# Kernel optimization log

Measured on AMD Instinct MI355X. Metric: run time of the kernel, lower is better.

The kernel has to match this reference:

```python
import jax, jax.numpy as jnp
import numpy as np

NUM_HEADS = 10
FEATURE_DIM = 200
HEAD_DIM = FEATURE_DIM // NUM_HEADS  # 20


def setup_inputs() -> dict:
    key = jax.random.key(0)
    k0, k1, k2, k3 = jax.random.split(key, 4)
    B, H, F, D = 128, 128, 8, FEATURE_DIM
    x = jax.random.normal(k0, (B, H, F, D), dtype=jnp.float32)
    wq = 0.02 * jax.random.normal(k1, (D, NUM_HEADS * HEAD_DIM), dtype=jnp.float32)
    wk = 0.02 * jax.random.normal(k2, (D, NUM_HEADS * HEAD_DIM), dtype=jnp.float32)
    wv = 0.02 * jax.random.normal(k3, (D, NUM_HEADS * HEAD_DIM), dtype=jnp.float32)
    return {"history_embedding_vec": x, "wq": wq, "wk": wk, "wv": wv}


def reference(history_embedding_vec, wq, wk, wv):
    B, H, F, D = history_embedding_vec.shape  # (batch, history_len, feature_num, feature_dim)
    nh, hd = NUM_HEADS, HEAD_DIM
    # Faithful to torch .view: a raw row-major memory reshape (mixes dims, not a transpose)
    x = history_embedding_vec.reshape(B * F, H, D)
    q = (x @ wq).reshape(B * F, H, nh, hd).transpose(0, 2, 1, 3)  # (BF, nh, H, hd)
    k = (x @ wk).reshape(B * F, H, nh, hd).transpose(0, 2, 1, 3)
    v = (x @ wv).reshape(B * F, H, nh, hd).transpose(0, 2, 1, 3)
    scale = 1.0 / jnp.sqrt(jnp.float32(hd))
    scores = jnp.einsum('bhsd,bhtd->bhst', q, k) * scale  # (BF, nh, H, H)
    attention_weights = jax.nn.softmax(scores, axis=-1)
    out = jnp.einsum('bhst,bhtd->bshd', attention_weights, v).reshape(B, F, H, nh * hd)
    # Original re-uses wq (reshaped, but nh*hd == D so identical) for output projection
    out = (out @ wq.reshape(nh * hd, D)).reshape(B, F, H, D)
    return (attention_weights, out)
```

## Files before the change

### kernel.cpp

```cpp
#include <hip/hip_runtime.h>

typedef __bf16 bf16x8 __attribute__((ext_vector_type(8)));
typedef float f32x4 __attribute__((ext_vector_type(4)));

__device__ __forceinline__ unsigned short f2b(float f) {
  union { float f; unsigned u; } v; v.f = f;
  unsigned u = v.u;
  u = (u + 0x7fffu + ((u >> 16) & 1u)) >> 16;
  return (unsigned short)u;
}
__device__ __forceinline__ void lds_load16(void* lds, const void* g) {
  __builtin_amdgcn_global_load_lds(
      (const __attribute__((address_space(1))) unsigned int*)g,
      (__attribute__((address_space(3))) unsigned int*)lds, 16, 0, 0);
}

__global__ __launch_bounds__(256) void cvt_x_kernel(const float* __restrict__ x,
                                                    unsigned short* __restrict__ xb) {
  size_t i = (size_t)blockIdx.x * 256 + threadIdx.x;
  const float4* xp = (const float4*)(x + i * 8);
  float4 a = xp[0], b = xp[1];
  uint4 o;
  o.x = (unsigned)f2b(a.x) | ((unsigned)f2b(a.y) << 16);
  o.y = (unsigned)f2b(a.z) | ((unsigned)f2b(a.w) << 16);
  o.z = (unsigned)f2b(b.x) | ((unsigned)f2b(b.y) << 16);
  o.w = (unsigned)f2b(b.z) | ((unsigned)f2b(b.w) << 16);
  *(uint4*)(xb + i * 8) = o;
}

__global__ __launch_bounds__(256) void build_wt_kernel(const float* __restrict__ wq,
                                                       const float* __restrict__ wk,
                                                       const float* __restrict__ wv,
                                                       unsigned short* __restrict__ wt) {
  int i = blockIdx.x * 256 + threadIdx.x;
  int n = i / 224, k = i - n * 224;
  float val = 0.f;
  if (n < 600 && k < 200) {
    const float* src = (n < 200) ? wq : ((n < 400) ? wk : wv);
    val = src[k * 200 + (n % 200)];
  }
  wt[i] = f2b(val);
}

__global__ __launch_bounds__(256, 3) void gemm_kernel(
    const unsigned short* __restrict__ A, long Astride,
    const unsigned short* __restrict__ Bt,
    unsigned short* __restrict__ Cb, float* __restrict__ Cf,
    long Cstride, int Ncols, int permuteQKV) {
  __shared__ unsigned short sA[2][128 * 32];
  __shared__ unsigned short sB[2][128 * 32];
  int nb = blockIdx.x, mb = blockIdx.y;
  long mBase = (long)mb * 128;
  int nBase = nb * 128;
  int tid = threadIdx.x;
  int lane = tid & 63, w = tid >> 6;
  int wm = w & 1, wn = w >> 1;
  int frow = lane & 15, fch = lane >> 4;

  int chunk0 = w * 64 + lane;
  int row0 = chunk0 >> 2, cs0 = chunk0 & 3;
  int cg0 = cs0 ^ ((row0 >> 1) & 3);
  int chunk1 = 256 + chunk0;
  int row1 = chunk1 >> 2, cs1 = chunk1 & 3;
  int cg1 = cs1 ^ ((row1 >> 1) & 3);

  f32x4 acc[4][4] = {};

#define STAGE(buf, k0)                                                          \
  do {                                                                          \
    lds_load16(&sA[buf][(w * 64) * 8], A + (mBase + row0) * Astride + (k0) + cg0 * 8); \
    lds_load16(&sB[buf][(w * 64) * 8], Bt + (long)(nBase + row0) * 224 + (k0) + cg0 * 8); \
    lds_load16(&sA[buf][(256 + w * 64) * 8], A + (mBase + row1) * Astride + (k0) + cg1 * 8); \
    lds_load16(&sB[buf][(256 + w * 64) * 8], Bt + (long)(nBase + row1) * 224 + (k0) + cg1 * 8); \
  } while (0)

  STAGE(0, 0);
  __syncthreads();

  int cur = 0;
  for (int kk = 0; kk < 7; ++kk) {
    if (kk < 6) STAGE(cur ^ 1, (kk + 1) * 32);
    bf16x8 fa[4], fb[4];
    for (int i = 0; i < 4; i++) {
      int r = wm * 64 + i * 16 + frow;
      fa[i] = *(const bf16x8*)&sA[cur][r * 32 + (fch ^ ((r >> 1) & 3)) * 8];
    }
    for (int j = 0; j < 4; j++) {
      int r = wn * 64 + j * 16 + frow;
      fb[j] = *(const bf16x8*)&sB[cur][r * 32 + (fch ^ ((r >> 1) & 3)) * 8];
    }
    for (int i = 0; i < 4; i++)
      for (int j = 0; j < 4; j++)
        acc[i][j] = __builtin_amdgcn_mfma_f32_16x16x32_bf16(fa[i], fb[j], acc[i][j], 0, 0, 0);
    __syncthreads();
    cur ^= 1;
  }
#undef STAGE

  int rbase = (lane >> 4) * 4;
  int cN = lane & 15;
  for (int j = 0; j < 4; j++) {
    int n = nBase + wn * 64 + j * 16 + cN;
    if (n < Ncols) {
      long cidx = n;
      if (permuteQKV) {
        int t = n / 200; int rem = n - t * 200;
        int hh = rem / 20; int d = rem - hh * 20;
        cidx = hh * 60 + t * 20 + d;
      }
      for (int i = 0; i < 4; i++) {
        long rowg = mBase + wm * 64 + i * 16 + rbase;
        for (int r = 0; r < 4; r++) {
          long off = (rowg + r) * Cstride + cidx;
          if (Cb) Cb[off] = f2b(acc[i][j][r]);
          else __builtin_nontemporal_store(acc[i][j][r], &Cf[off]);
        }
      }
    }
  }
}

__global__ __launch_bounds__(256, 3) void attn_kernel(
    const unsigned short* __restrict__ qkv,
    float* __restrict__ attn_out,
    unsigned short* __restrict__ out_pre) {
  __shared__ __align__(16) unsigned short smem[21760];
  unsigned short* sS = smem;
  unsigned short* sQ = smem;
  unsigned short* sK = smem + 5120;
  unsigned short* sV = smem + 17408;

  int blk = blockIdx.x;
  int bf = blk / 10, h = blk - bf * 10;
  int tid = threadIdx.x, lane = tid & 63, wid = tid >> 6;
  long rowBase = (long)bf * 128;
  int frow = lane & 15, fk = (lane >> 4) * 8;
  int g4 = (lane >> 4) * 4;

  {
    uint4 z = {0, 0, 0, 0};
    uint4* p = (uint4*)smem;
    for (int i = tid; i < 1280; i += 256) p[i] = z;
  }
  __syncthreads();

  for (int c = tid; c < 1920; c += 256) {
    int row = c / 15, j = c - row * 15;
    const unsigned short* g = qkv + (rowBase + row) * 600 + h * 60 + j * 4;
    ushort4 d = *(const ushort4*)g;
    int tile = j / 5, jj = j - tile * 5;
    if (tile < 2) {
      *(ushort4*)((tile == 0 ? sQ : sK) + row * 40 + jj * 4) = d;
    } else {
      int d0 = jj * 4;
      sV[(d0 + 0) * 136 + row] = d.x;
      sV[(d0 + 1) * 136 + row] = d.y;
      sV[(d0 + 2) * 136 + row] = d.z;
      sV[(d0 + 3) * 136 + row] = d.w;
    }
  }
  __syncthreads();

  f32x4 acc[2][8] = {};
  {
    bf16x8 qf0 = *(const bf16x8*)&sQ[(wid * 32 + frow) * 40 + fk];
    bf16x8 qf1 = *(const bf16x8*)&sQ[(wid * 32 + 16 + frow) * 40 + fk];
#pragma unroll
    for (int j = 0; j < 8; j++) {
      bf16x8 kf = *(const bf16x8*)&sK[(j * 16 + frow) * 40 + fk];
      acc[0][j] = __builtin_amdgcn_mfma_f32_16x16x32_bf16(qf0, kf, acc[0][j], 0, 0, 0);
      acc[1][j] = __builtin_amdgcn_mfma_f32_16x16x32_bf16(qf1, kf, acc[1][j], 0, 0, 0);
    }
  }
  __syncthreads();

  const float scale = 0.22360679774997896f;
  long attnBase = (long)blk * 16384;
#pragma unroll
  for (int i = 0; i < 2; i++) {
#pragma unroll
    for (int r = 0; r < 4; r++) {
      float m = acc[i][0][r];
#pragma unroll
      for (int j = 1; j < 8; j++) m = fmaxf(m, acc[i][j][r]);
      m = fmaxf(m, __shfl_xor(m, 1, 64));
      m = fmaxf(m, __shfl_xor(m, 2, 64));
      m = fmaxf(m, __shfl_xor(m, 4, 64));
      m = fmaxf(m, __shfl_xor(m, 8, 64));
      float s = 0.f;
#pragma unroll
      for (int j = 0; j < 8; j++) {
        float e = __expf((acc[i][j][r] - m) * scale);
        acc[i][j][r] = e;
        s += e;
      }
      s += __shfl_xor(s, 1, 64);
      s += __shfl_xor(s, 2, 64);
      s += __shfl_xor(s, 4, 64);
      s += __shfl_xor(s, 8, 64);
      float inv = 1.0f / s;
      int srow = wid * 32 + i * 16 + g4 + r;
      float* gout = attn_out + attnBase + (long)srow * 128 + frow;
      unsigned short* lout = sS + srow * 136 + frow;
#pragma unroll
      for (int j = 0; j < 8; j++) {
        float wgt = acc[i][j][r] * inv;
        __builtin_nontemporal_store(wgt, &gout[j * 16]);
        lout[j * 16] = f2b(wgt);
      }
    }
  }

  f32x4 accO[2][2] = {};
  int m0 = wid * 32;
#pragma unroll
  for (int ks = 0; ks < 4; ks++) {
    bf16x8 pf0 = *(const bf16x8*)&sS[(m0 + frow) * 136 + ks * 32 + fk];
    bf16x8 pf1 = *(const bf16x8*)&sS[(m0 + 16 + frow) * 136 + ks * 32 + fk];
    bf16x8 vf0 = *(const bf16x8*)&sV[frow * 136 + ks * 32 + fk];
    bf16x8 vf1 = *(const bf16x8*)&sV[(16 + frow) * 136 + ks * 32 + fk];
    accO[0][0] = __builtin_amdgcn_mfma_f32_16x16x32_bf16(pf0, vf0, accO[0][0], 0, 0, 0);
    accO[0][1] = __builtin_amdgcn_mfma_f32_16x16x32_bf16(pf0, vf1, accO[0][1], 0, 0, 0);
    accO[1][0] = __builtin_amdgcn_mfma_f32_16x16x32_bf16(pf1, vf0, accO[1][0], 0, 0, 0);
    accO[1][1] = __builtin_amdgcn_mfma_f32_16x16x32_bf16(pf1, vf1, accO[1][1], 0, 0, 0);
  }
#pragma unroll
  for (int i = 0; i < 2; i++)
#pragma unroll
    for (int j = 0; j < 2; j++) {
      int d = j * 16 + frow;
      if (d < 20) {
        int srow = m0 + i * 16 + g4;
#pragma unroll
        for (int r = 0; r < 4; r++)
          out_pre[(rowBase + srow + r) * 200 + h * 20 + d] = f2b(accO[i][j][r]);
      }
    }
}

extern "C" void kernel_launch(void* const* d_in, const int* in_sizes, int n_in,
                              void* d_out, int out_size, void* d_ws, size_t ws_size,
                              hipStream_t stream) {
  const float* x  = (const float*)d_in[0];
  const float* wq = (const float*)d_in[1];
  const float* wk = (const float*)d_in[2];
  const float* wv = (const float*)d_in[3];
  float* out = (float*)d_out;

  char* ws = (char*)d_ws;
  unsigned short* xb      = (unsigned short*)ws;
  unsigned short* wt      = (unsigned short*)(ws + 52428800);
  unsigned short* qkv     = (unsigned short*)(ws + 52428800 + 286720);
  unsigned short* out_pre = xb;

  cvt_x_kernel<<<12800, 256, 0, stream>>>(x, xb);
  build_wt_kernel<<<560, 256, 0, stream>>>(wq, wk, wv, wt);
  gemm_kernel<<<dim3(5, 1024), 256, 0, stream>>>(xb, 200, wt, qkv, nullptr, 600, 600, 1);
  attn_kernel<<<10240, 256, 0, stream>>>(qkv, out, out_pre);
  gemm_kernel<<<dim3(2, 1024), 256, 0, stream>>>(out_pre, 200, wt, nullptr,
                                                 out + 167772160L, 200, 200, 0);
}
```

Measured before the change: 1.134 ms.

## Shrink attention LDS footprint for higher occupancy and remap GEMM blocks across XCDs

The attention kernel's shared memory shrinks from about 43KB to 27KB. Q/K rows are now stored with a 24-element stride, with padding lanes masked in registers instead of zero-filling LDS. The softmax probability tile is written to LDS in two 64-column halves that reuse the Q/K region, and the occupancy hint rises from 3 to 4 blocks per CU. The GEMM launches switch to a 1D grid whose block index is remapped so consecutive tiles land on the same XCD, aiming for better L2 reuse. The risks are extra register work for the masking and an extra LDS write phase, with no added synchronisation between the two P halves.

```diff
diff --git a/kernel.cpp b/kernel.cpp
--- a/kernel.cpp
+++ b/kernel.cpp
@@ -13,6 +13,11 @@
   __builtin_amdgcn_global_load_lds(
       (const __attribute__((address_space(1))) unsigned int*)g,
       (__attribute__((address_space(3))) unsigned int*)lds, 16, 0, 0);
+}
+__device__ __forceinline__ bf16x8 maskpad(bf16x8 v, int fch) {
+  if (fch >= 2) { v[4] = (__bf16)0.f; v[5] = (__bf16)0.f; v[6] = (__bf16)0.f; v[7] = (__bf16)0.f; }
+  if (fch == 3) { v[0] = (__bf16)0.f; v[1] = (__bf16)0.f; v[2] = (__bf16)0.f; v[3] = (__bf16)0.f; }
+  return v;
 }
 
 __global__ __launch_bounds__(256) void cvt_x_kernel(const float* __restrict__ x,
@@ -46,10 +51,12 @@
     const unsigned short* __restrict__ A, long Astride,
     const unsigned short* __restrict__ Bt,
     unsigned short* __restrict__ Cb, float* __restrict__ Cf,
-    long Cstride, int Ncols, int permuteQKV) {
+    long Cstride, int Ncols, int permuteQKV, int NB) {
   __shared__ unsigned short sA[2][128 * 32];
   __shared__ unsigned short sB[2][128 * 32];
-  int nb = blockIdx.x, mb = blockIdx.y;
+  int cpx = gridDim.x >> 3;
+  int g = ((blockIdx.x & 7) * cpx) + (blockIdx.x >> 3);
+  int mb = g / NB, nb = g - mb * NB;
   long mBase = (long)mb * 128;
   int nBase = nb * 128;
   int tid = threadIdx.x;
@@ -120,29 +127,23 @@
   }
 }
 
-__global__ __launch_bounds__(256, 3) void attn_kernel(
+__global__ __launch_bounds__(256, 4) void attn_kernel(
     const unsigned short* __restrict__ qkv,
     float* __restrict__ attn_out,
     unsigned short* __restrict__ out_pre) {
-  __shared__ __align__(16) unsigned short smem[21760];
+  __shared__ __align__(16) unsigned short smem[13568];
+  unsigned short* sQ = smem;
+  unsigned short* sK = smem + 3072;
   unsigned short* sS = smem;
-  unsigned short* sQ = smem;
-  unsigned short* sK = smem + 5120;
-  unsigned short* sV = smem + 17408;
+  unsigned short* sV = smem + 9216;
 
   int blk = blockIdx.x;
   int bf = blk / 10, h = blk - bf * 10;
   int tid = threadIdx.x, lane = tid & 63, wid = tid >> 6;
   long rowBase = (long)bf * 128;
-  int frow = lane & 15, fk = (lane >> 4) * 8;
-  int g4 = (lane >> 4) * 4;
-
-  {
-    uint4 z = {0, 0, 0, 0};
-    uint4* p = (uint4*)smem;
-    for (int i = tid; i < 1280; i += 256) p[i] = z;
-  }
-  __syncthreads();
+  int frow = lane & 15, fch = lane >> 4, fk = fch * 8;
+  int g4 = fch * 4;
+  int m0 = wid * 32;
 
   for (int c = tid; c < 1920; c += 256) {
     int row = c / 15, j = c - row * 15;
@@ -150,7 +151,7 @@
     ushort4 d = *(const ushort4*)g;
     int tile = j / 5, jj = j - tile * 5;
     if (tile < 2) {
-      *(ushort4*)((tile == 0 ? sQ : sK) + row * 40 + jj * 4) = d;
+      *(ushort4*)((tile == 0 ? sQ : sK) + row * 24 + jj * 4) = d;
     } else {
       int d0 = jj * 4;
       sV[(d0 + 0) * 136 + row] = d.x;
@@ -163,11 +164,11 @@
 
   f32x4 acc[2][8] = {};
   {
-    bf16x8 qf0 = *(const bf16x8*)&sQ[(wid * 32 + frow) * 40 + fk];
-    bf16x8 qf1 = *(const bf16x8*)&sQ[(wid * 32 + 16 + frow) * 40 + fk];
+    bf16x8 qf0 = maskpad(*(const bf16x8*)&sQ[(m0 + frow) * 24 + fk], fch);
+    bf16x8 qf1 = maskpad(*(const bf16x8*)&sQ[(m0 + 16 + frow) * 24 + fk], fch);
 #pragma unroll
     for (int j = 0; j < 8; j++) {
-      bf16x8 kf = *(const bf16x8*)&sK[(j * 16 + frow) * 40 + fk];
+      bf16x8 kf = maskpad(*(const bf16x8*)&sK[(j * 16 + frow) * 24 + fk], fch);
       acc[0][j] = __builtin_amdgcn_mfma_f32_16x16x32_bf16(qf0, kf, acc[0][j], 0, 0, 0);
       acc[1][j] = __builtin_amdgcn_mfma_f32_16x16x32_bf16(qf1, kf, acc[1][j], 0, 0, 0);
     }
@@ -199,30 +200,45 @@
       s += __shfl_xor(s, 4, 64);
       s += __shfl_xor(s, 8, 64);
       float inv = 1.0f / s;
-      int srow = wid * 32 + i * 16 + g4 + r;
+      int srow = m0 + i * 16 + g4 + r;
       float* gout = attn_out + attnBase + (long)srow * 128 + frow;
-      unsigned short* lout = sS + srow * 136 + frow;
+      unsigned short* lout = sS + srow * 72 + frow;
 #pragma unroll
       for (int j = 0; j < 8; j++) {
         float wgt = acc[i][j][r] * inv;
+        acc[i][j][r] = wgt;
         __builtin_nontemporal_store(wgt, &gout[j * 16]);
-        lout[j * 16] = f2b(wgt);
-      }
+      }
+#pragma unroll
+      for (int j = 0; j < 4; j++) lout[j * 16] = f2b(acc[i][j][r]);
     }
   }
 
   f32x4 accO[2][2] = {};
-  int m0 = wid * 32;
-#pragma unroll
-  for (int ks = 0; ks < 4; ks++) {
-    bf16x8 pf0 = *(const bf16x8*)&sS[(m0 + frow) * 136 + ks * 32 + fk];
-    bf16x8 pf1 = *(const bf16x8*)&sS[(m0 + 16 + frow) * 136 + ks * 32 + fk];
-    bf16x8 vf0 = *(const bf16x8*)&sV[frow * 136 + ks * 32 + fk];
-    bf16x8 vf1 = *(const bf16x8*)&sV[(16 + frow) * 136 + ks * 32 + fk];
-    accO[0][0] = __builtin_amdgcn_mfma_f32_16x16x32_bf16(pf0, vf0, accO[0][0], 0, 0, 0);
-    accO[0][1] = __builtin_amdgcn_mfma_f32_16x16x32_bf16(pf0, vf1, accO[0][1], 0, 0, 0);
-    accO[1][0] = __builtin_amdgcn_mfma_f32_16x16x32_bf16(pf1, vf0, accO[1][0], 0, 0, 0);
-    accO[1][1] = __builtin_amdgcn_mfma_f32_16x16x32_bf16(pf1, vf1, accO[1][1], 0, 0, 0);
+#pragma unroll
+  for (int p = 0; p < 2; p++) {
+    if (p == 1) {
+#pragma unroll
+      for (int i = 0; i < 2; i++)
+#pragma unroll
+        for (int r = 0; r < 4; r++) {
+          int srow = m0 + i * 16 + g4 + r;
+          unsigned short* lout = sS + srow * 72 + frow;
+#pragma unroll
+          for (int j = 0; j < 4; j++) lout[j * 16] = f2b(acc[i][4 + j][r]);
+        }
+    }
+#pragma unroll
+    for (int ks = 0; ks < 2; ks++) {
+      bf16x8 pf0 = *(const bf16x8*)&sS[(m0 + frow) * 72 + ks * 32 + fk];
+      bf16x8 pf1 = *(const bf16x8*)&sS[(m0 + 16 + frow) * 72 + ks * 32 + fk];
+      bf16x8 vf0 = *(const bf16x8*)&sV[frow * 136 + p * 64 + ks * 32 + fk];
+      bf16x8 vf1 = *(const bf16x8*)&sV[(16 + frow) * 136 + p * 64 + ks * 32 + fk];
+      accO[0][0] = __builtin_amdgcn_mfma_f32_16x16x32_bf16(pf0, vf0, accO[0][0], 0, 0, 0);
+      accO[0][1] = __builtin_amdgcn_mfma_f32_16x16x32_bf16(pf0, vf1, accO[0][1], 0, 0, 0);
+      accO[1][0] = __builtin_amdgcn_mfma_f32_16x16x32_bf16(pf1, vf0, accO[1][0], 0, 0, 0);
+      accO[1][1] = __builtin_amdgcn_mfma_f32_16x16x32_bf16(pf1, vf1, accO[1][1], 0, 0, 0);
+    }
   }
 #pragma unroll
   for (int i = 0; i < 2; i++)
@@ -255,8 +271,8 @@
 
   cvt_x_kernel<<<12800, 256, 0, stream>>>(x, xb);
   build_wt_kernel<<<560, 256, 0, stream>>>(wq, wk, wv, wt);
-  gemm_kernel<<<dim3(5, 1024), 256, 0, stream>>>(xb, 200, wt, qkv, nullptr, 600, 600, 1);
+  gemm_kernel<<<5120, 256, 0, stream>>>(xb, 200, wt, qkv, nullptr, 600, 600, 1, 5);
   attn_kernel<<<10240, 256, 0, stream>>>(qkv, out, out_pre);
-  gemm_kernel<<<dim3(2, 1024), 256, 0, stream>>>(out_pre, 200, wt, nullptr,
-                                                 out + 167772160L, 200, 200, 0);
-}
+  gemm_kernel<<<2048, 256, 0, stream>>>(out_pre, 200, wt, nullptr,
+                                        out + 167772160L, 200, 200, 0, 2);
+}
```

Measured after the change: 1.070 ms. -5.6%, faster.
